# Kernel optimization log

Measured on AMD Instinct MI355X. Metric: run time of the kernel, lower is better.

## Reference

```python
import jax, jax.numpy as jnp
import numpy as np

EPS = 1e-8
THRESHOLD = 0.2

def setup_inputs() -> dict:
    key = jax.random.key(0)
    k1, k2 = jax.random.split(key)
    N, D, H = 8192, 256, 2
    x = jax.random.normal(k1, (N, D), dtype=jnp.float32)
    # per-head elementwise metric weight (MetricCalcLayer.weight, xavier-uniform init)
    bound = float(np.sqrt(6.0 / (1 + D)))
    w = jax.random.uniform(k2, (H, D), dtype=jnp.float32, minval=-bound, maxval=bound)
    K = 81  # int(N * 0.01), resolved top-k count per row
    return {"x": x, "w": w, "K": K}

def reference(x, w, K):
    # x: [N, D], w: [H, D]
    H = w.shape[0]
    N = x.shape[0]
    wx = x[None, :, :] * w[:, None, :]                       # [H, N, D]
    norms = jnp.linalg.norm(wx, axis=-1, keepdims=True)      # [H, N, 1]
    wn = wx / jnp.maximum(norms, EPS)                        # normalized per head
    # sum of per-head cosine similarity matrices, averaged over heads
    sim = jnp.einsum('hnd,hmd->nm', wn, wn) / H              # [N, N]
    # threshold (reverse=False): zero out entries below threshold
    sim = jnp.where(sim < THRESHOLD, jnp.zeros_like(sim), sim)
    # top-k per row -> scatter ones into a mask, multiply
    _, idx = jax.lax.top_k(sim, K)                           # [N, K]
    mask = jnp.zeros_like(sim).at[jnp.arange(N)[:, None], idx].set(1.0)
    return sim * mask
```

## Files before the change

### kernel.cpp

```cpp
#include <hip/hip_runtime.h>
#include <hip/hip_bf16.h>
#include <stdint.h>

#define NROWS 8192
#define DIM   256
#define KDIM  512
#define THRESH 0.2f
#define MARGIN 0.005f
#define BLK_FIX_CAP 512
#define TOPK_CAP 4096

typedef __bf16 bf16x8 __attribute__((ext_vector_type(8)));
typedef float  f32x4  __attribute__((ext_vector_type(4)));
typedef float  f32x2  __attribute__((ext_vector_type(2)));

__device__ __forceinline__ void gload16(const void* g, void* l) {
  __builtin_amdgcn_global_load_lds(
      (const __attribute__((address_space(1))) uint32_t*)g,
      (__attribute__((address_space(3))) uint32_t*)l,
      16, 0, 0);
}

__global__ __launch_bounds__(256) void prep_k(const float* __restrict__ x,
                                              const float* __restrict__ w,
                                              ushort* __restrict__ z,
                                              int* __restrict__ cnt) {
  const int n = blockIdx.x;
  const int d = threadIdx.x;
  if (d == 0) cnt[n] = 0;
  const float xv = x[(size_t)n * DIM + d];
  const float p0 = xv * w[d];
  const float p1 = xv * w[DIM + d];
  float s0 = p0 * p0, s1 = p1 * p1;
  #pragma unroll
  for (int off = 32; off > 0; off >>= 1) {
    s0 += __shfl_down(s0, off);
    s1 += __shfl_down(s1, off);
  }
  __shared__ float red0[4], red1[4];
  const int wv = d >> 6, ln = d & 63;
  if (ln == 0) { red0[wv] = s0; red1[wv] = s1; }
  __syncthreads();
  const float t0 = red0[0] + red0[1] + red0[2] + red0[3];
  const float t1 = red1[0] + red1[1] + red1[2] + red1[3];
  const float inv0 = 0.70710678118654752f / fmaxf(sqrtf(t0), 1e-8f);
  const float inv1 = 0.70710678118654752f / fmaxf(sqrtf(t1), 1e-8f);
  __hip_bfloat16 z0 = __float2bfloat16(p0 * inv0);
  __hip_bfloat16 z1 = __float2bfloat16(p1 * inv1);
  z[(size_t)n * KDIM + d]       = *(ushort*)&z0;
  z[(size_t)n * KDIM + DIM + d] = *(ushort*)&z1;
}

__global__ __launch_bounds__(256) void sim_gemm(const ushort* __restrict__ z,
                                               const float* __restrict__ x,
                                               const float* __restrict__ w,
                                               float* __restrict__ out,
                                               int* __restrict__ cnt) {
  const int u = blockIdx.x;
  int bm = (int)((129.0 - sqrt(129.0 * 129.0 - 8.0 * (double)u)) * 0.5);
  if (bm > 63) bm = 63;
  while (bm * (129 - bm) / 2 > u) --bm;
  while ((bm + 1) * (129 - (bm + 1)) / 2 <= u) ++bm;
  const int bn = bm + (u - bm * (129 - bm) / 2);
  const bool offd = (bm != bn);

  __shared__ __align__(16) char smem[33280];
  ushort* ASb = (ushort*)smem;
  ushort* BSb = (ushort*)(smem + 16384);
  auto T2 = (float (*)[32][130])smem;
  __shared__ int cntA[128], cntB[128];
  __shared__ uint32_t fix_loc[BLK_FIX_CAP];
  __shared__ int fix_loc_n;

  const int t = threadIdx.x;
  const int rowA = bm * 128, rowB = bn * 128;
  const int wv = t >> 6, lane = t & 63;
  const int wr = wv >> 1, wc = wv & 1;

  f32x4 acc[4][4];
  #pragma unroll
  for (int i = 0; i < 4; ++i)
    #pragma unroll
    for (int j = 0; j < 4; ++j) acc[i][j] = (f32x4)0.f;

  int aoff[4], boff[4];
  #pragma unroll
  for (int mi = 0; mi < 4; ++mi) {
    const int ar = wr * 64 + mi * 16 + (lane & 15);
    const int sw = (lane >> 4) ^ ((ar >> 1) & 3);
    aoff[mi] = ar * 32 + sw * 8;
  }
  #pragma unroll
  for (int ni = 0; ni < 4; ++ni) {
    const int br = wc * 64 + ni * 16 + (lane & 15);
    const int sw = (lane >> 4) ^ ((br >> 1) & 3);
    boff[ni] = br * 32 + sw * 8;
  }

  if (t < 128) { cntA[t] = 0; cntB[t] = 0; }
  if (t == 0) fix_loc_n = 0;

  const int i0 = t, r0 = i0 >> 2, s0_ = i0 & 3, cs0 = s0_ ^ ((r0 >> 1) & 3);
  const int i1 = t + 256, r1 = i1 >> 2, s1_ = i1 & 3, cs1 = s1_ ^ ((r1 >> 1) & 3);
  const ushort* zA0 = z + (size_t)(rowA + r0) * KDIM + cs0 * 8;
  const ushort* zB0 = z + (size_t)(rowB + r0) * KDIM + cs0 * 8;
  const ushort* zA1 = z + (size_t)(rowA + r1) * KDIM + cs1 * 8;
  const ushort* zB1 = z + (size_t)(rowB + r1) * KDIM + cs1 * 8;

  gload16(zA0,      ASb + (size_t)i0 * 8);
  gload16(zB0,      BSb + (size_t)i0 * 8);
  gload16(zA1,      ASb + (size_t)i1 * 8);
  gload16(zB1,      BSb + (size_t)i1 * 8);
  gload16(zA0 + 32, ASb + 4096 + (size_t)i0 * 8);
  gload16(zB0 + 32, BSb + 4096 + (size_t)i0 * 8);
  gload16(zA1 + 32, ASb + 4096 + (size_t)i1 * 8);
  gload16(zB1 + 32, BSb + 4096 + (size_t)i1 * 8);

  int cur = 0;
#define KSTEP(VMWAIT, STAGE_KB)                                                   \
  {                                                                               \
    asm volatile("s_waitcnt " VMWAIT ::: "memory");                               \
    __builtin_amdgcn_s_barrier();                                                 \
    __builtin_amdgcn_sched_barrier(0);                                            \
    const ushort* Ac = ASb + cur * 4096;                                          \
    const ushort* Bc = BSb + cur * 4096;                                          \
    bf16x8 af[4], bfv[4];                                                         \
    _Pragma("unroll")                                                             \
    for (int mi = 0; mi < 4; ++mi) af[mi] = *(const bf16x8*)(Ac + aoff[mi]);      \
    _Pragma("unroll")                                                             \
    for (int ni = 0; ni < 4; ++ni) bfv[ni] = *(const bf16x8*)(Bc + boff[ni]);     \
    asm volatile("s_waitcnt lgkmcnt(0)" ::: "memory");                            \
    __builtin_amdgcn_sched_barrier(0);                                            \
    __builtin_amdgcn_s_barrier();                                                 \
    __builtin_amdgcn_sched_barrier(0);                                            \
    if ((STAGE_KB) >= 0) {                                                        \
      const int kb = (STAGE_KB);                                                  \
      ushort* An = ASb + cur * 4096;                                              \
      ushort* Bn = BSb + cur * 4096;                                              \
      gload16(zA0 + kb, An + (size_t)i0 * 8);                                     \
      gload16(zB0 + kb, Bn + (size_t)i0 * 8);                                     \
      gload16(zA1 + kb, An + (size_t)i1 * 8);                                     \
      gload16(zB1 + kb, Bn + (size_t)i1 * 8);                                     \
    }                                                                             \
    _Pragma("unroll")                                                             \
    for (int mi = 0; mi < 4; ++mi)                                                \
      _Pragma("unroll")                                                           \
      for (int ni = 0; ni < 4; ++ni)                                              \
        acc[mi][ni] = __builtin_amdgcn_mfma_f32_16x16x32_bf16(af[mi], bfv[ni],    \
                                                              acc[mi][ni], 0, 0, 0); \
    cur ^= 1;                                                                     \
  }

  for (int kt = 0; kt < 14; ++kt) KSTEP("vmcnt(4)", (kt + 2) * 32);
  KSTEP("vmcnt(4)", -1);
  KSTEP("vmcnt(0)", -1);
#undef KSTEP

  #pragma unroll
  for (int mi = 0; mi < 4; ++mi) {
    #pragma unroll
    for (int ni = 0; ni < 4; ++ni) {
      const f32x4 v = acc[mi][ni];
      const int lc = wc * 64 + ni * 16 + (lane & 15);
      const int gc = rowB + lc;
      const int lrbase = wr * 64 + mi * 16 + (lane >> 4) * 4;
      #pragma unroll
      for (int r = 0; r < 4; ++r) {
        const float val = v[r];
        const int lr = lrbase + r;
        out[(size_t)(rowA + lr) * NROWS + gc] = (val < THRESH) ? 0.0f : val;
        if (val >= THRESH - MARGIN) {
          atomicAdd(&cntA[lr], 1);
          if (offd) atomicAdd(&cntB[lc], 1);
          if (val < THRESH + MARGIN) {
            const int p = atomicAdd(&fix_loc_n, 1);
            if (p < BLK_FIX_CAP) fix_loc[p] = (uint32_t)(rowA + lr) * NROWS + gc;
          }
        }
      }
    }
  }

  if (offd) {
    #pragma unroll
    for (int p = 0; p < 2; ++p) {
      __syncthreads();
      {
        const int c = p + 2 * wc;
        #pragma unroll
        for (int ni2 = 0; ni2 < 2; ++ni2) {
          const int ni = p * 2 + ni2;
          const int tc = ni2 * 16 + (lane & 15);
          #pragma unroll
          for (int mi = 0; mi < 4; ++mi) {
            const int lrb = wr * 64 + mi * 16 + (lane >> 4) * 4;
            #pragma unroll
            for (int r = 0; r < 4; ++r) T2[wc][tc][lrb + r] = acc[mi][ni][r];
          }
        }
      }
      __syncthreads();
      #pragma unroll
      for (int h = 0; h < 2; ++h) {
        const int c = p + 2 * h;
        #pragma unroll
        for (int it = 0; it < 8; ++it) {
          const int j = it * 4 + wv;
          const int i = (t & 63) * 2;
          f32x2 v2 = *(const f32x2*)&T2[h][j][i];
          v2.x = (v2.x < THRESH) ? 0.0f : v2.x;
          v2.y = (v2.y < THRESH) ? 0.0f : v2.y;
          __builtin_nontemporal_store(v2,
              (f32x2*)&out[(size_t)(rowB + c * 32 + j) * NROWS + rowA + i]);
        }
      }
    }
  }
  __syncthreads();

  {
    const int nf = (fix_loc_n < BLK_FIX_CAP) ? fix_loc_n : BLK_FIX_CAP;
    for (int e = wv; e < nf; e += 4) {
      const uint32_t f = fix_loc[e];
      const int r = (int)(f / NROWS), c = (int)(f % NROWS);
      double dot0 = 0, dot1 = 0, nr0 = 0, nr1 = 0, nc0 = 0, nc1 = 0;
      #pragma unroll
      for (int i2 = 0; i2 < DIM / 64; ++i2) {
        const int i = i2 * 64 + lane;
        const double w0 = (double)w[i],              w1 = (double)w[DIM + i];
        const double xr = (double)x[(size_t)r * DIM + i];
        const double xc = (double)x[(size_t)c * DIM + i];
        const double pr0 = xr * w0, pc0 = xc * w0;
        const double pr1 = xr * w1, pc1 = xc * w1;
        dot0 += pr0 * pc0; nr0 += pr0 * pr0; nc0 += pc0 * pc0;
        dot1 += pr1 * pc1; nr1 += pr1 * pr1; nc1 += pc1 * pc1;
      }
      #pragma unroll
      for (int off = 32; off > 0; off >>= 1) {
        dot0 += __shfl_down(dot0, off); nr0 += __shfl_down(nr0, off); nc0 += __shfl_down(nc0, off);
        dot1 += __shfl_down(dot1, off); nr1 += __shfl_down(nr1, off); nc1 += __shfl_down(nc1, off);
      }
      if (lane == 0) {
        const double s0 = dot0 / (fmax(sqrt(nr0), 1e-8) * fmax(sqrt(nc0), 1e-8));
        const double s1 = dot1 / (fmax(sqrt(nr1), 1e-8) * fmax(sqrt(nc1), 1e-8));
        const double sim = 0.5 * (s0 + s1);
        const float res = (sim < (double)THRESH) ? 0.0f : (float)sim;
        out[(size_t)r * NROWS + c] = res;
        out[(size_t)c * NROWS + r] = res;
      }
    }
  }

  if (t < 128) {
    if (cntA[t] > 0) atomicAdd(&cnt[rowA + t], cntA[t]);
    if (offd && cntB[t] > 0) atomicAdd(&cnt[rowB + t], cntB[t]);
  }
}

__global__ __launch_bounds__(256) void topk_fix(float* __restrict__ out,
                                                const int* __restrict__ cnt,
                                                const int* __restrict__ Kp) {
  const int row = blockIdx.x;
  const int K = Kp[0];
  if (cnt[row] <= K) return;

  __shared__ float vals[TOPK_CAP];
  __shared__ int   idxs[TOPK_CAP];
  __shared__ int   num;
  if (threadIdx.x == 0) num = 0;
  __syncthreads();
  for (int j = threadIdx.x; j < NROWS; j += 256) {
    const float v = out[(size_t)row * NROWS + j];
    if (v != 0.0f) {
      const int p = atomicAdd(&num, 1);
      if (p < TOPK_CAP) { vals[p] = v; idxs[p] = j; }
    }
  }
  __syncthreads();
  const int c = (num < TOPK_CAP) ? num : TOPK_CAP;
  for (int p = threadIdx.x; p < c; p += 256) {
    const float v = vals[p];
    const int  id = idxs[p];
    int rank = 0;
    for (int q = 0; q < c; ++q) {
      const float u = vals[q];
      rank += (u > v) || (u == v && idxs[q] < id);
    }
    if (rank >= K) out[(size_t)row * NROWS + id] = 0.0f;
  }
}

extern "C" void kernel_launch(void* const* d_in, const int* in_sizes, int n_in,
                              void* d_out, int out_size, void* d_ws, size_t ws_size,
                              hipStream_t stream) {
  const float* x  = (const float*)d_in[0];
  const float* w  = (const float*)d_in[1];
  const int*   Kp = (const int*)d_in[2];
  float* out = (float*)d_out;

  char* ws = (char*)d_ws;
  ushort* z   = (ushort*)ws;
  int*    cnt = (int*)(ws + (size_t)NROWS * KDIM * 2);

  prep_k<<<NROWS, 256, 0, stream>>>(x, w, z, cnt);
  sim_gemm<<<2080, 256, 0, stream>>>(z, x, w, out, cnt);
  topk_fix<<<NROWS, 256, 0, stream>>>(out, cnt, Kp);
}
```

Baseline: 128.0 us.

## Memset output then write only above-threshold similarities sparsely, dropping transpose staging

The output is now zeroed up front with a memset, and the GEMM epilogue writes only entries at or above the threshold, together with their mirrored transpose, as scattered stores. This removes the LDS-staged coalesced transpose write and the dense zero stores from the GEMM kernel. In exchange the full 256MB output gets a separate memset pass, and the surviving mirrored stores are strided and uncoalesced. How much this saves depends on how sparse the thresholded matrix is.

After: 152.2 us. 18.9% more time.

```diff
diff --git a/kernel.cpp b/kernel.cpp
--- a/kernel.cpp
+++ b/kernel.cpp
@@ -12,7 +12,6 @@
 
 typedef __bf16 bf16x8 __attribute__((ext_vector_type(8)));
 typedef float  f32x4  __attribute__((ext_vector_type(4)));
-typedef float  f32x2  __attribute__((ext_vector_type(2)));
 
 __device__ __forceinline__ void gload16(const void* g, void* l) {
   __builtin_amdgcn_global_load_lds(
@@ -64,10 +63,9 @@
   const int bn = bm + (u - bm * (129 - bm) / 2);
   const bool offd = (bm != bn);
 
-  __shared__ __align__(16) char smem[33280];
+  __shared__ __align__(16) char smem[32768];
   ushort* ASb = (ushort*)smem;
   ushort* BSb = (ushort*)(smem + 16384);
-  auto T2 = (float (*)[32][130])smem;
   __shared__ int cntA[128], cntB[128];
   __shared__ uint32_t fix_loc[BLK_FIX_CAP];
   __shared__ int fix_loc_n;
@@ -168,50 +166,18 @@
       for (int r = 0; r < 4; ++r) {
         const float val = v[r];
         const int lr = lrbase + r;
-        out[(size_t)(rowA + lr) * NROWS + gc] = (val < THRESH) ? 0.0f : val;
+        const int gr = rowA + lr;
+        if (val >= THRESH) {
+          out[(size_t)gr * NROWS + gc] = val;
+          if (offd) out[(size_t)gc * NROWS + gr] = val;
+        }
         if (val >= THRESH - MARGIN) {
           atomicAdd(&cntA[lr], 1);
           if (offd) atomicAdd(&cntB[lc], 1);
           if (val < THRESH + MARGIN) {
             const int p = atomicAdd(&fix_loc_n, 1);
-            if (p < BLK_FIX_CAP) fix_loc[p] = (uint32_t)(rowA + lr) * NROWS + gc;
+            if (p < BLK_FIX_CAP) fix_loc[p] = (uint32_t)gr * NROWS + gc;
           }
-        }
-      }
-    }
-  }
-
-  if (offd) {
-    #pragma unroll
-    for (int p = 0; p < 2; ++p) {
-      __syncthreads();
-      {
-        const int c = p + 2 * wc;
-        #pragma unroll
-        for (int ni2 = 0; ni2 < 2; ++ni2) {
-          const int ni = p * 2 + ni2;
-          const int tc = ni2 * 16 + (lane & 15);
-          #pragma unroll
-          for (int mi = 0; mi < 4; ++mi) {
-            const int lrb = wr * 64 + mi * 16 + (lane >> 4) * 4;
-            #pragma unroll
-            for (int r = 0; r < 4; ++r) T2[wc][tc][lrb + r] = acc[mi][ni][r];
-          }
-        }
-      }
-      __syncthreads();
-      #pragma unroll
-      for (int h = 0; h < 2; ++h) {
-        const int c = p + 2 * h;
-        #pragma unroll
-        for (int it = 0; it < 8; ++it) {
-          const int j = it * 4 + wv;
-          const int i = (t & 63) * 2;
-          f32x2 v2 = *(const f32x2*)&T2[h][j][i];
-          v2.x = (v2.x < THRESH) ? 0.0f : v2.x;
-          v2.y = (v2.y < THRESH) ? 0.0f : v2.y;
-          __builtin_nontemporal_store(v2,
-              (f32x2*)&out[(size_t)(rowB + c * 32 + j) * NROWS + rowA + i]);
         }
       }
     }
@@ -302,6 +268,7 @@
   ushort* z   = (ushort*)ws;
   int*    cnt = (int*)(ws + (size_t)NROWS * KDIM * 2);
 
+  hipMemsetAsync(out, 0, (size_t)NROWS * NROWS * sizeof(float), stream);
   prep_k<<<NROWS, 256, 0, stream>>>(x, w, z, cnt);
   sim_gemm<<<2080, 256, 0, stream>>>(z, x, w, out, cnt);
   topk_fix<<<NROWS, 256, 0, stream>>>(out, cnt, Kp);
```
